# Kernel tuning notes

Hardware: AMD Instinct MI355X
Metric: run time of the kernel (lower is better)

Reference implementation:

```python
import jax, jax.numpy as jnp
import numpy as np


def _conv(x, w, b, stride, pad):
    y = jax.lax.conv_general_dilated(
        x, w, window_strides=(stride, stride),
        padding=((pad, pad), (pad, pad)),
        dimension_numbers=('NCHW', 'OIHW', 'NCHW'))
    return y + b[None, :, None, None]


def setup_inputs() -> dict:
    key = jax.random.key(0)
    ks = jax.random.split(key, 10)
    B, C, H, W = 4, 3, 256, 256
    HID, D, K = 128, 32, 65536
    s = 0.05
    return {
        'x': jax.random.normal(ks[0], (B, C, H, W), dtype=jnp.float32),
        'w1': jax.random.normal(ks[1], (HID, C, 4, 4), dtype=jnp.float32) * s,
        'b1': jnp.zeros((HID,), dtype=jnp.float32),
        'w2': jax.random.normal(ks[2], (HID, HID, 4, 4), dtype=jnp.float32) * s,
        'b2': jnp.zeros((HID,), dtype=jnp.float32),
        'w3': jax.random.normal(ks[3], (HID, HID, 4, 4), dtype=jnp.float32) * s,
        'b3': jnp.zeros((HID,), dtype=jnp.float32),
        'w4': jax.random.normal(ks[4], (D, HID, 3, 3), dtype=jnp.float32) * s,
        'b4': jnp.zeros((D,), dtype=jnp.float32),
        'codebook': jax.random.normal(ks[5], (K, D), dtype=jnp.float32),
    }


def reference(x, w1, b1, w2, b2, w3, b3, w4, b4, codebook):
    z = jax.nn.relu(_conv(x, w1, b1, 2, 1))
    z = jax.nn.relu(_conv(z, w2, b2, 2, 1))
    z = jax.nn.relu(_conv(z, w3, b3, 2, 1))
    z = _conv(z, w4, b4, 1, 1)                 # [B, D, h, w]
    z = jnp.transpose(z, (0, 2, 3, 1))          # [B, h, w, D]
    B, h, w, D = z.shape
    zf = z.reshape(-1, D)                        # [N, D]
    # pairwise squared distances: ||z||^2 + ||e||^2 - 2 z.e
    d = (jnp.sum(zf * zf, axis=1, keepdims=True)
         + jnp.sum(codebook * codebook, axis=1)[None, :]
         - 2.0 * jnp.matmul(zf, codebook.T))    # [N, K]
    idx = jnp.argmin(d, axis=1)                  # [N]
    z_q = codebook[idx].reshape(B, h, w, D)
    return idx.reshape(B, h, w), z_q
```

## Files before the change

kernel.cpp:

```cpp
#include <hip/hip_runtime.h>
#include <cfloat>

typedef float f32x4 __attribute__((ext_vector_type(4)));
typedef _Float16 h8 __attribute__((ext_vector_type(8)));

static __device__ __forceinline__ unsigned umin_(unsigned a, unsigned b) { return a < b ? a : b; }
static __device__ __forceinline__ unsigned umax_(unsigned a, unsigned b) { return a > b ? a : b; }
static __device__ __forceinline__ unsigned med3_(unsigned a, unsigned b, unsigned c) {
    unsigned d;
    asm("v_med3_u32 %0, %1, %2, %3" : "=v"(d) : "v"(a), "v"(b), "v"(c));
    return d;
}

static __device__ __forceinline__ void gl_lds16(const h8* g, h8* s) {
    __builtin_amdgcn_global_load_lds(
        (const __attribute__((address_space(1))) unsigned int*)g,
        (__attribute__((address_space(3))) unsigned int*)s, 16, 0, 0);
}


__global__ __launch_bounds__(256)
void zero_b_k(_Float16* p0, _Float16* p1, _Float16* p2, _Float16* p3,
              _Float16* p4, _Float16* p5) {
    const int s = blockIdx.y;
    _Float16* p; int np, P;
    switch (s) {
        case 0: p = p0; np = 16; P = 66; break;
        case 1: p = p1; np = 16; P = 66; break;
        case 2: p = p2; np = 16; P = 34; break;
        case 3: p = p3; np = 16; P = 34; break;
        case 4: p = p4; np = 4;  P = 34; break;
        default: p = p5; np = 4; P = 34; break;
    }
    const int plane = blockIdx.x;
    if (plane >= np) return;
    _Float16* pl = p + (size_t)plane * P * P * 128;
    const int rowN = P * 128;
    for (int i = threadIdx.x; i < rowN; i += 256) {
        pl[i] = (_Float16)0.f;
        pl[(size_t)(P - 1) * rowN + i] = (_Float16)0.f;
        const int r = i >> 7, c = i & 127;
        pl[(size_t)r * rowN + c] = (_Float16)0.f;
        pl[(size_t)r * rowN + (P - 1) * 128 + c] = (_Float16)0.f;
    }
}

__global__ __launch_bounds__(256)
void conv1_k(const float* __restrict__ in, const float* __restrict__ w,
             const float* __restrict__ bias,
             _Float16* __restrict__ Dh, _Float16* __restrict__ Dl) {
    __shared__ float tile[3][34 * 36];
    const int tid = threadIdx.x;
    const int tx = tid & 15, ty = tid >> 4;
    const int bx = blockIdx.x & 7, by = blockIdx.x >> 3;
    const int oc0 = blockIdx.y * 8;
    const int b = blockIdx.z;
    const int ox = bx * 16 + tx, oy = by * 16 + ty;
    const int ix0 = bx * 32 - 1, iy0 = by * 32 - 1;

    for (int f = tid; f < 3 * 34 * 34; f += 256) {
        const int ic = f / 1156, r2 = f % 1156;
        const int r = r2 / 34, c = r2 % 34;
        const int iy = iy0 + r, ix = ix0 + c;
        float v = ((unsigned)iy < 256u && (unsigned)ix < 256u)
                      ? in[((size_t)(b * 3 + ic) * 256 + iy) * 256 + ix] : 0.f;
        tile[ic][r * 36 + c] = v;
    }
    __syncthreads();

    float acc[8];
#pragma unroll
    for (int j = 0; j < 8; ++j) acc[j] = 0.f;
#pragma unroll
    for (int ic = 0; ic < 3; ++ic) {
#pragma unroll
        for (int kh = 0; kh < 4; ++kh) {
            const float2* p = (const float2*)&tile[ic][(2 * ty + kh) * 36 + 2 * tx];
            const float2 r0 = p[0], r1 = p[1];
            const float tap[4] = {r0.x, r0.y, r1.x, r1.y};
#pragma unroll
            for (int kw = 0; kw < 4; ++kw)
#pragma unroll
                for (int j = 0; j < 8; ++j)
                    acc[j] = fmaf(tap[kw], w[((oc0 + j) * 3 + ic) * 16 + kh * 4 + kw], acc[j]);
        }
    }

    h8 hv, lv;
#pragma unroll
    for (int j = 0; j < 8; ++j) {
        float r = fmaxf(acc[j] + bias[oc0 + j], 0.f);
        _Float16 h = (_Float16)r;
        hv[j] = h;
        lv[j] = (_Float16)((r - (float)h) * 2048.f);
    }
    const size_t di = (((size_t)((b * 2 + (oy & 1)) * 2 + (ox & 1)) * 66 + 1 + (oy >> 1)) * 66
                       + 1 + (ox >> 1)) * 128 + oc0;
    *(h8*)(Dh + di) = hv;
    *(h8*)(Dl + di) = lv;
}

__global__ __launch_bounds__(256)
void pack3_k(const float* __restrict__ w2, const float* __restrict__ w3,
             const float* __restrict__ w4,
             h8* __restrict__ B2h, h8* __restrict__ B2l,
             h8* __restrict__ B3h, h8* __restrict__ B3l,
             h8* __restrict__ B4h, h8* __restrict__ B4l) {
    const float* w; h8 *Bh, *Bl; int T, NT, KHKW;
    switch (blockIdx.y) {
        case 0:  w = w2; Bh = B2h; Bl = B2l; T = 16; NT = 8; KHKW = 16; break;
        case 1:  w = w3; Bh = B3h; Bl = B3l; T = 16; NT = 8; KHKW = 16; break;
        default: w = w4; Bh = B4h; Bl = B4l; T = 9;  NT = 2; KHKW = 9;  break;
    }
    const int idx = blockIdx.x * 256 + threadIdx.x;
    if (idx >= T * 4 * NT * 64) return;
    const int lane = idx & 63;
    int r = idx >> 6;
    const int nt = r % NT; r /= NT;
    const int ks = r & 3;  r >>= 2;
    const int t = r;
    const int oc = nt * 16 + (lane & 15);
    const int icb = ks * 32 + (lane >> 4) * 8;
    h8 hv, lv;
#pragma unroll
    for (int j = 0; j < 8; ++j) {
        const float v = w[(size_t)(oc * 128 + icb + j) * KHKW + t];
        _Float16 h = (_Float16)v;
        hv[j] = h;
        lv[j] = (_Float16)((v - (float)h) * 2048.f);
    }
    Bh[idx] = hv;
    Bl[idx] = lv;
}

template<int WN, bool SPLIT>
__global__ __launch_bounds__(256)
void gemmS2_k(const _Float16* __restrict__ Ah, const _Float16* __restrict__ Al,
              const h8* __restrict__ Bh, const h8* __restrict__ Bl,
              const float* __restrict__ bias,
              _Float16* __restrict__ Dh, _Float16* __restrict__ Dl,
              int OW, int OH, int PP, int dPP) {
    constexpr int NW_N = 8 / WN;
    constexpr int NW_M = 4 / NW_N;
    __shared__ h8 lH[2048];
    __shared__ h8 lL[2048];

    const int tid = threadIdx.x, wid = tid >> 6, l = tid & 63;
    const int nq = wid % NW_N, mi = wid / NW_N;
    const int mt = blockIdx.x * NW_M + mi;
    const int mpr = OW >> 4, mpi = OH * mpr;
    const int b = mt / mpi;
    const int rem = mt % mpi;
    const int oy = rem / mpr, ox = (rem % mpr) << 4;
    const int laneA = (l & 15) * 128 + (l >> 4) * 8;

    f32x4 a1[WN], am[WN];
#pragma unroll
    for (int s = 0; s < WN; ++s) {
        a1[s] = (f32x4){0.f, 0.f, 0.f, 0.f};
        am[s] = (f32x4){0.f, 0.f, 0.f, 0.f};
    }

#pragma unroll 1
    for (int t = 0; t < 16; ++t) {
        {
            const h8* sh = Bh + (size_t)t * 2048 + wid * 512 + l;
            const h8* sl = Bl + (size_t)t * 2048 + wid * 512 + l;
#pragma unroll
            for (int i = 0; i < 8; ++i)
                gl_lds16(sh + i * 64, &lH[wid * 512 + i * 64]);
#pragma unroll
            for (int i = 0; i < 8; ++i)
                gl_lds16(sl + i * 64, &lL[wid * 512 + i * 64]);
        }
        const int kh = t >> 2, kw = t & 3;
        const int dy = (kh - 1) >> 1, dx = (kw - 1) >> 1;
        const int py = (kh - 1) & 1, px = (kw - 1) & 1;
        const int pidx = (b * 2 + py) * 2 + px;
        const size_t abase = ((size_t)(pidx * PP + (oy + dy + 1)) * PP
                              + (ox + dx + 1)) * 128 + laneA;
        h8 avh[4], avl[4];
#pragma unroll
        for (int ks = 0; ks < 4; ++ks) {
            avh[ks] = *(const h8*)(Ah + abase + ks * 32);
            avl[ks] = *(const h8*)(Al + abase + ks * 32);
        }
        __syncthreads();
#pragma unroll
        for (int ks = 0; ks < 4; ++ks) {
#pragma unroll
            for (int s = 0; s < WN; ++s) {
                const h8 bvh = lH[(ks * 8 + nq * WN + s) * 64 + l];
                const h8 bvl = lL[(ks * 8 + nq * WN + s) * 64 + l];
                a1[s] = __builtin_amdgcn_mfma_f32_16x16x32_f16(avh[ks], bvh, a1[s], 0, 0, 0);
                am[s] = __builtin_amdgcn_mfma_f32_16x16x32_f16(avh[ks], bvl, am[s], 0, 0, 0);
                am[s] = __builtin_amdgcn_mfma_f32_16x16x32_f16(avl[ks], bvh, am[s], 0, 0, 0);
            }
        }
        __syncthreads();
    }

#pragma unroll
    for (int s = 0; s < WN; ++s) {
        const int oc = (nq * WN + s) * 16 + (l & 15);
        const float bv = bias[oc];
#pragma unroll
        for (int i = 0; i < 4; ++i) {
            const int row = (l >> 4) * 4 + i;
            float v = fmaf(am[s][i], 4.8828125e-4f, a1[s][i]);
            v = fmaxf(v + bv, 0.f);
            _Float16 h = (_Float16)v;
            _Float16 lo = (_Float16)((v - (float)h) * 2048.f);
            const int oxp = ox + row;
            size_t di;
            if constexpr (SPLIT) {
                di = (((size_t)((b * 2 + (oy & 1)) * 2 + (oxp & 1)) * dPP
                       + 1 + (oy >> 1)) * dPP + 1 + (oxp >> 1)) * 128 + oc;
            } else {
                di = ((size_t)(b * dPP + 1 + oy) * dPP + 1 + oxp) * 128 + oc;
            }
            Dh[di] = h;
            Dl[di] = lo;
        }
    }
}

template<int S, bool FIN, int WPN, int MT>
__global__ __launch_bounds__(256)
void gemm_k(const _Float16* __restrict__ Ah, const _Float16* __restrict__ Al,
            const h8* __restrict__ Bh, const h8* __restrict__ Bl,
            float* __restrict__ part, const float* __restrict__ bias,
            _Float16* __restrict__ Dh, _Float16* __restrict__ Dl,
            int OW, int OH, int PP, int NT, int TPS, int M, int N, int dPP) {
    const int tid = threadIdx.x, wid = tid >> 6, l = tid & 63;
    const int ntb = wid % WPN;
    const int mt0 = (blockIdx.x * (4 / WPN) + wid / WPN) * MT;
    const int sp = blockIdx.y;
    const int mpr = OW >> 4, mpi = OH * mpr;
    const int laneA = (l & 15) * 128 + (l >> 4) * 8;

    int bmt[MT], oymt[MT], oxmt[MT];
#pragma unroll
    for (int m = 0; m < MT; ++m) {
        const int mt = mt0 + m;
        bmt[m] = mt / mpi;
        const int rem = mt % mpi;
        oymt[m] = rem / mpr;
        oxmt[m] = (rem % mpr) << 4;
    }

    f32x4 a1[MT][2], am[MT][2];
#pragma unroll
    for (int m = 0; m < MT; ++m)
#pragma unroll
        for (int s = 0; s < 2; ++s) {
            a1[m][s] = (f32x4){0.f, 0.f, 0.f, 0.f};
            am[m][s] = (f32x4){0.f, 0.f, 0.f, 0.f};
        }

    const int t0 = sp * TPS, t1 = t0 + TPS;
#pragma unroll 2
    for (int t = t0; t < t1; ++t) {
        int dy, dx, pidx[MT];
        if constexpr (S == 2) {
            const int kh = t >> 2, kw = t & 3;
            dy = (kh - 1) >> 1; dx = (kw - 1) >> 1;
            const int py = (kh - 1) & 1, px = (kw - 1) & 1;
#pragma unroll
            for (int m = 0; m < MT; ++m) pidx[m] = (bmt[m] * 2 + py) * 2 + px;
        } else {
            dy = t / 3 - 1; dx = t % 3 - 1;
#pragma unroll
            for (int m = 0; m < MT; ++m) pidx[m] = bmt[m];
        }
        const _Float16* pAh[MT]; const _Float16* pAl[MT];
#pragma unroll
        for (int m = 0; m < MT; ++m) {
            const size_t base = ((size_t)(pidx[m] * PP + (oymt[m] + dy + 1)) * PP
                                 + (oxmt[m] + dx + 1)) * 128 + laneA;
            pAh[m] = Ah + base;
            pAl[m] = Al + base;
        }
        const size_t bbase = ((size_t)(t * 4) * NT + ntb * 2) * 64 + l;
#pragma unroll
        for (int ks = 0; ks < 4; ++ks) {
            h8 avh[MT], avl[MT];
#pragma unroll
            for (int m = 0; m < MT; ++m) {
                avh[m] = *(const h8*)(pAh[m] + ks * 32);
                avl[m] = *(const h8*)(pAl[m] + ks * 32);
            }
#pragma unroll
            for (int s = 0; s < 2; ++s) {
                const h8 bvh = Bh[bbase + (size_t)ks * NT * 64 + s * 64];
                const h8 bvl = Bl[bbase + (size_t)ks * NT * 64 + s * 64];
#pragma unroll
                for (int m = 0; m < MT; ++m) {
                    a1[m][s] = __builtin_amdgcn_mfma_f32_16x16x32_f16(avh[m], bvh, a1[m][s], 0, 0, 0);
                    am[m][s] = __builtin_amdgcn_mfma_f32_16x16x32_f16(avh[m], bvl, am[m][s], 0, 0, 0);
                    am[m][s] = __builtin_amdgcn_mfma_f32_16x16x32_f16(avl[m], bvh, am[m][s], 0, 0, 0);
                }
            }
        }
    }

#pragma unroll
    for (int m = 0; m < MT; ++m) {
        const int mt = mt0 + m;
#pragma unroll
        for (int s = 0; s < 2; ++s) {
            const int oc = ntb * 32 + s * 16 + (l & 15);
#pragma unroll
            for (int i = 0; i < 4; ++i) {
                const int row = (l >> 4) * 4 + i;
                float v = fmaf(am[m][s][i], 4.8828125e-4f, a1[m][s][i]);
                if (!FIN) {
                    part[((size_t)sp * M + mt * 16 + row) * N + oc] = v;
                } else {
                    v = fmaxf(v + bias[oc], 0.f);
                    _Float16 h = (_Float16)v;
                    _Float16 lo = (_Float16)((v - (float)h) * 2048.f);
                    const int ox = oxmt[m] + row;
                    const int oy = oymt[m], b = bmt[m];
                    const size_t di = (((size_t)((b * 2 + (oy & 1)) * 2 + (ox & 1)) * dPP
                                        + 1 + (oy >> 1)) * dPP + 1 + (ox >> 1)) * 128 + oc;
                    Dh[di] = h;
                    Dl[di] = lo;
                }
            }
        }
    }
}

__global__ __launch_bounds__(256)
void fin4_k(const float* __restrict__ part, const float* __restrict__ bias,
            float* __restrict__ zz, h8* __restrict__ zh, h8* __restrict__ zl) {
    const int t = blockIdx.x * 256 + threadIdx.x;
    const int m = t >> 2, g8 = (t & 3) * 8;
    float v[8];
#pragma unroll
    for (int j = 0; j < 8; ++j) v[j] = bias[g8 + j];
#pragma unroll
    for (int sp = 0; sp < 3; ++sp) {
        const float4* p = (const float4*)(part + ((size_t)sp * 4096 + m) * 32 + g8);
        float4 x0 = p[0], x1 = p[1];
        v[0] += x0.x; v[1] += x0.y; v[2] += x0.z; v[3] += x0.w;
        v[4] += x1.x; v[5] += x1.y; v[6] += x1.z; v[7] += x1.w;
    }
    float4* dst = (float4*)(zz + (size_t)m * 32 + g8);
    dst[0] = make_float4(v[0], v[1], v[2], v[3]);
    dst[1] = make_float4(v[4], v[5], v[6], v[7]);
    h8 hv, lv;
#pragma unroll
    for (int j = 0; j < 8; ++j) {
        const float mv = -2.f * v[j];
        _Float16 h = (_Float16)mv;
        hv[j] = h;
        lv[j] = (_Float16)(mv - (float)h);
    }
    const int idx = (m >> 4) * 64 + (m & 15) + (t & 3) * 16;
    zh[idx] = hv;
    zl[idx] = lv;
}

#define VQ_NSPLIT 64
#define VQ_KSPC   1024
#define VQ_NCHUNK 8
#define VQ_TAU_S  102.4f
#define VQ_ABS_S  524288.0f
#define VQ_QT     4

__global__ __launch_bounds__(256)
void split_cb_k(const float* __restrict__ cb, h8* __restrict__ cbh, h8* __restrict__ cbl,
                float* __restrict__ cbn2, float* __restrict__ cbn_raw,
                unsigned* __restrict__ counter) {
    const int c = blockIdx.x * 256 + threadIdx.x;
    const float4* p = (const float4*)(cb + (size_t)c * 32);
    float e[32];
    float s = 0.f;
#pragma unroll
    for (int i = 0; i < 8; ++i) {
        float4 v = p[i];
        e[i*4+0] = v.x; e[i*4+1] = v.y; e[i*4+2] = v.z; e[i*4+3] = v.w;
        s += v.x*v.x + v.y*v.y + v.z*v.z + v.w*v.w;
    }
    cbn_raw[c] = s;
    cbn2[c]    = (s + 512.0f) * 2048.0f;
    const int base = (c >> 4) * 64 + (c & 15);
#pragma unroll
    for (int g = 0; g < 4; ++g) {
        h8 hv, lv;
#pragma unroll
        for (int j = 0; j < 8; ++j) {
            float v = e[g*8 + j];
            _Float16 h = (_Float16)v;
            hv[j] = (_Float16)((float)h * 2048.0f);
            lv[j] = (_Float16)((v - (float)h) * 2048.0f);
        }
        cbh[base + g*16] = hv;
        cbl[base + g*16] = lv;
    }
    if (c == 0) *counter = 0u;
}

__global__ __launch_bounds__(256, 4)
void vq_mfma_k(const h8* __restrict__ zh, const h8* __restrict__ zl,
               const uint4* __restrict__ cbh, const uint4* __restrict__ cbl,
               const float* __restrict__ cbn2,
               unsigned* __restrict__ pb1, unsigned* __restrict__ pb2,
               unsigned* __restrict__ pcol) {
    __shared__ uint4 lH[2][512];
    __shared__ uint4 lL[2][512];
    __shared__ float lN[2][128];

    const int tid = threadIdx.x;
    const int w = tid >> 6, ln = tid & 63;
    const int split = blockIdx.y;
    const int qt0 = (blockIdx.x * 4 + w) * VQ_QT;

    h8 azh[VQ_QT], azl[VQ_QT];
#pragma unroll
    for (int qq = 0; qq < VQ_QT; ++qq) {
        azh[qq] = zh[(qt0 + qq) * 64 + ln];
        azl[qq] = zl[(qt0 + qq) * 64 + ln];
    }

    unsigned b1[VQ_QT][4], b2[VQ_QT][4];
#pragma unroll
    for (int qq = 0; qq < VQ_QT; ++qq)
#pragma unroll
        for (int i = 0; i < 4; ++i) { b1[qq][i] = 0x7F800000u; b2[qq][i] = 0x7F800000u; }

    const int fbase = split * (VQ_KSPC * 4);
    const int nbase = split * VQ_KSPC;

    {
        uint4 h0 = cbh[fbase + tid], h1 = cbh[fbase + 256 + tid];
        uint4 l0 = cbl[fbase + tid], l1 = cbl[fbase + 256 + tid];
        lH[0][tid] = h0; lH[0][tid + 256] = h1;
        lL[0][tid] = l0; lL[0][tid + 256] = l1;
        if (tid < 128) lN[0][tid] = cbn2[nbase + tid];
    }
    __syncthreads();

    for (int ci = 0; ci < VQ_NCHUNK; ++ci) {
        const int cur = ci & 1;
        const bool more = (ci + 1 < VQ_NCHUNK);
        uint4 nh0, nh1, nl0, nl1; float nn = 0.f;
        if (more) {
            const int nb = fbase + (ci + 1) * 512;
            nh0 = cbh[nb + tid]; nh1 = cbh[nb + 256 + tid];
            nl0 = cbl[nb + tid]; nl1 = cbl[nb + 256 + tid];
            if (tid < 128) nn = cbn2[nbase + (ci + 1) * 128 + tid];
        }

        const unsigned tcb = (unsigned)(ci * 8);
#pragma unroll
        for (int t = 0; t < 8; ++t) {
            const h8 bh = *reinterpret_cast<const h8*>(&lH[cur][t*64 + ln]);
            const h8 bl = *reinterpret_cast<const h8*>(&lL[cur][t*64 + ln]);
            const float nv = lN[cur][t*16 + (ln & 15)];
            f32x4 nvv = {nv, nv, nv, nv};
            const unsigned tc = tcb + t;
#pragma unroll
            for (int qq = 0; qq < VQ_QT; ++qq) {
                f32x4 acc;
                acc = __builtin_amdgcn_mfma_f32_16x16x32_f16(azh[qq], bh, nvv, 0, 0, 0);
                acc = __builtin_amdgcn_mfma_f32_16x16x32_f16(azh[qq], bl, acc, 0, 0, 0);
                acc = __builtin_amdgcn_mfma_f32_16x16x32_f16(azl[qq], bh, acc, 0, 0, 0);
#pragma unroll
                for (int i = 0; i < 4; ++i) {
                    const unsigned k0 = (__float_as_uint(acc[i]) & 0xFFFFFF00u) | tc;
                    b2[qq][i] = med3_(b1[qq][i], b2[qq][i], k0);
                    b1[qq][i] = umin_(b1[qq][i], k0);
                }
            }
        }

        if (more) {
            const int nxt = cur ^ 1;
            lH[nxt][tid] = nh0; lH[nxt][tid + 256] = nh1;
            lL[nxt][tid] = nl0; lL[nxt][tid + 256] = nl1;
            if (tid < 128) lN[nxt][tid] = nn;
        }
        __syncthreads();
    }

#pragma unroll
    for (int qq = 0; qq < VQ_QT; ++qq) {
#pragma unroll
        for (int i = 0; i < 4; ++i) {
            unsigned v1 = b1[qq][i], v2 = b2[qq][i], cv = (unsigned)(ln & 15);
#pragma unroll
            for (int m = 1; m < 16; m <<= 1) {
                unsigned o1 = __shfl_xor(v1, m, 64);
                unsigned o2 = __shfl_xor(v2, m, 64);
                unsigned oc = __shfl_xor(cv, m, 64);
                unsigned nb2 = umin_(umin_(v2, o2), umax_(v1, o1));
                if (o1 < v1) cv = oc;
                v1 = umin_(v1, o1); v2 = nb2;
            }
            if ((ln & 15) == 0) {
                const int q = (qt0 + qq) * 16 + (ln >> 4) * 4 + i;
                pb1[(size_t)q * VQ_NSPLIT + split] = v1;
                pb2[(size_t)q * VQ_NSPLIT + split] = v2;
                pcol[(size_t)q * VQ_NSPLIT + split] = cv;
            }
        }
    }
}

__global__ __launch_bounds__(256)
void combine_k(const unsigned* __restrict__ pb1, const unsigned* __restrict__ pb2,
               const unsigned* __restrict__ pcol,
               unsigned* __restrict__ coarse, unsigned* __restrict__ flags,
               unsigned* __restrict__ list, unsigned* __restrict__ counter) {
    const int q = blockIdx.x * 256 + threadIdx.x;
    unsigned B1 = 0x7F800000u, B2 = 0x7F800000u, PAY = 0u;
#pragma unroll 4
    for (int s = 0; s < VQ_NSPLIT; ++s) {
        unsigned a1 = pb1[(size_t)q * VQ_NSPLIT + s];
        unsigned a2 = pb2[(size_t)q * VQ_NSPLIT + s];
        unsigned ac = pcol[(size_t)q * VQ_NSPLIT + s];
        unsigned nb2 = umin_(umin_(B2, a2), umax_(B1, a1));
        if (a1 < B1) PAY = ((unsigned)s << 4) | ac;
        B1 = umin_(B1, a1); B2 = nb2;
    }
    const unsigned tile = B1 & 0xFFu;
    const unsigned code = (PAY >> 4) * VQ_KSPC + tile * 16 + (PAY & 15u);
    const float f1 = __uint_as_float(B1 & 0xFFFFFF00u);
    const float f2 = __uint_as_float(B2 & 0xFFFFFF00u);
    const int fl = (f2 - f1 < VQ_TAU_S) || (f1 < VQ_ABS_S);
    coarse[q] = code;
    flags[q] = (unsigned)fl;
    if (fl) { unsigned p = atomicAdd(counter, 1u); list[p] = q; }
}

__global__ __launch_bounds__(256)
void guard_k(const float* __restrict__ cb, const float* __restrict__ cbn_raw,
             const float* __restrict__ zz, const unsigned* __restrict__ list,
             const unsigned* __restrict__ counter, float2* __restrict__ gpart) {
    __shared__ float lcb[256 * 36];
    __shared__ float lnr[256];
    __shared__ float2 red[4];
    __shared__ int ns;

    const int tid = threadIdx.x;
    const int w = tid >> 6, ln = tid & 63;
    const int bx = blockIdx.x;

    const float4* cb4 = (const float4*)cb;
#pragma unroll
    for (int it = 0; it < 8; ++it) {
        const int f = tid + it * 256;
        float4 v = cb4[(size_t)bx * 2048 + f];
        const int c = f >> 3, g = f & 7;
        *(float4*)&lcb[c * 36 + g * 4] = v;
    }
    lnr[tid] = cbn_raw[bx * 256 + tid];
    if (tid == 0) ns = (int)*(volatile unsigned*)counter;
    __syncthreads();

    for (int ii = blockIdx.y; ii < ns; ii += 8) {
        const int q = (int)list[ii];
        const float4* zq = (const float4*)(zz + (size_t)q * 32);
        float m2[32];
#pragma unroll
        for (int j = 0; j < 8; ++j) {
            float4 v = zq[j];
            m2[j*4+0] = -2.f*v.x; m2[j*4+1] = -2.f*v.y; m2[j*4+2] = -2.f*v.z; m2[j*4+3] = -2.f*v.w;
        }
        float d = lnr[tid];
#pragma unroll
        for (int j = 0; j < 8; ++j) {
            float4 e = *(const float4*)&lcb[tid * 36 + j * 4];
            d = fmaf(m2[j*4+0], e.x, d);
            d = fmaf(m2[j*4+1], e.y, d);
            d = fmaf(m2[j*4+2], e.z, d);
            d = fmaf(m2[j*4+3], e.w, d);
        }
        float bv = d; int bc = tid;
#pragma unroll
        for (int m = 1; m < 64; m <<= 1) {
            float ov = __shfl_xor(bv, m, 64);
            int   oi = __shfl_xor(bc, m, 64);
            if (ov < bv || (ov == bv && oi < bc)) { bv = ov; bc = oi; }
        }
        if (ln == 0) red[w] = make_float2(bv, (float)(bx * 256 + bc));
        __syncthreads();
        if (tid == 0) {
            float2 r = red[0];
#pragma unroll
            for (int k = 1; k < 4; ++k) {
                float2 o = red[k];
                if (o.x < r.x || (o.x == r.x && o.y < r.y)) r = o;
            }
            gpart[(size_t)q * 256 + bx] = r;
        }
        __syncthreads();
    }
}

__global__ __launch_bounds__(256)
void final_k(const unsigned* __restrict__ flags, const unsigned* __restrict__ coarse,
             const float2* __restrict__ gpart, const float* __restrict__ cb,
             float* __restrict__ out_idx, float* __restrict__ out_zq) {
    const int q = blockIdx.x * 256 + threadIdx.x;
    int bi;
    if (flags[q]) {
        float2 r = gpart[(size_t)q * 256];
        for (int b = 1; b < 256; ++b) {
            float2 o = gpart[(size_t)q * 256 + b];
            if (o.x < r.x || (o.x == r.x && o.y < r.y)) r = o;
        }
        bi = (int)r.y;
    } else {
        bi = (int)coarse[q];
    }
    out_idx[q] = (float)bi;
    const float4* src = (const float4*)(cb + (size_t)bi * 32);
    float4*       dst = (float4*)(out_zq + (size_t)q * 32);
#pragma unroll
    for (int i = 0; i < 8; ++i) dst[i] = src[i];
}

extern "C" void kernel_launch(void* const* d_in, const int* in_sizes, int n_in,
                              void* d_out, int out_size, void* d_ws, size_t ws_size,
                              hipStream_t stream) {
    const float* x  = (const float*)d_in[0];
    const float* w1 = (const float*)d_in[1];
    const float* b1 = (const float*)d_in[2];
    const float* w2 = (const float*)d_in[3];
    const float* b2 = (const float*)d_in[4];
    const float* w3 = (const float*)d_in[5];
    const float* b3 = (const float*)d_in[6];
    const float* w4 = (const float*)d_in[7];
    const float* b4 = (const float*)d_in[8];
    const float* cb = (const float*)d_in[9];
    float* out = (float*)d_out;

    float* ws = (float*)d_ws;
    _Float16* y1h = (_Float16*)ws;
    _Float16* y1l = (_Float16*)(ws + 4460544);
    _Float16* y2h = (_Float16*)(ws + 8921088);
    _Float16* y2l = (_Float16*)(ws + 10104832);
    _Float16* y3h = (_Float16*)(ws + 11288576);
    _Float16* y3l = (_Float16*)(ws + 11584512);
    float* zzp = ws + 11880448;
    h8* B2h = (h8*)(ws + 12011520);
    h8* B2l = (h8*)(ws + 12142592);
    h8* B3h = (h8*)(ws + 12273664);
    h8* B3l = (h8*)(ws + 12404736);
    h8* B4h = (h8*)(ws + 12535808);
    h8* B4l = (h8*)(ws + 12554240);
    float* part = ws + 12572672;
    h8*       cbh     = (h8*)ws;
    h8*       cbl     = (h8*)(ws + 1048576);
    h8*       zh      = (h8*)(ws + 2097152);
    h8*       zl      = (h8*)(ws + 2162688);
    float*    cbn2    = ws + 2228224;
    float*    cbn_raw = ws + 2293760;
    unsigned* pb1     = (unsigned*)(ws + 2359296);
    unsigned* pb2     = (unsigned*)(ws + 2621440);
    unsigned* pcol    = (unsigned*)(ws + 2883584);
    unsigned* coarse  = (unsigned*)(ws + 3145728);
    unsigned* flags   = (unsigned*)(ws + 3149824);
    unsigned* list    = (unsigned*)(ws + 3153920);
    unsigned* counter = (unsigned*)(ws + 3158016);
    float2*   gpart   = (float2*)(ws + 3158080);

    zero_b_k<<<dim3(16, 6), 256, 0, stream>>>(y1h, y1l, y2h, y2l, y3h, y3l);
    pack3_k<<<dim3(128, 3), 256, 0, stream>>>(w2, w3, w4, B2h, B2l, B3h, B3l, B4h, B4l);
    conv1_k<<<dim3(64, 16, 4), 256, 0, stream>>>(x, w1, b1, y1h, y1l);
    gemmS2_k<4, true><<<dim3(512), 256, 0, stream>>>(y1h, y1l, B2h, B2l, b2, y2h, y2l,
                                                     64, 64, 66, 34);
    gemmS2_k<2, false><<<dim3(256), 256, 0, stream>>>(y2h, y2l, B3h, B3l, b3, y3h, y3l,
                                                      32, 32, 34, 34);
    gemm_k<1, false, 1, 1><<<dim3(64, 3), 256, 0, stream>>>(y3h, y3l, B4h, B4l, part, nullptr, nullptr, nullptr,
                                                            32, 32, 34, 2, 3, 4096, 32, 0);
    fin4_k<<<64, 256, 0, stream>>>(part, b4, zzp, zh, zl);

    split_cb_k<<<256, 256, 0, stream>>>(cb, cbh, cbl, cbn2, cbn_raw, counter);
    vq_mfma_k <<<dim3(16, VQ_NSPLIT), 256, 0, stream>>>(zh, zl, (const uint4*)cbh, (const uint4*)cbl,
                                                        cbn2, pb1, pb2, pcol);
    combine_k <<<16,  256, 0, stream>>>(pb1, pb2, pcol, coarse, flags, list, counter);
    guard_k   <<<dim3(256, 8), 256, 0, stream>>>(cb, cbn_raw, zzp, list, counter, gpart);
    final_k   <<<16,  256, 0, stream>>>(flags, coarse, gpart, cb, out, out + 4096);
}
```

Measured before the change: 276.5 us.

## Double-buffer weight tiles in LDS and add M-tiling to stride-2 conv GEMM

The stride-2 convolution GEMM kernel now double-buffers the per-tap weight tiles in LDS, prefetching tap t+1 with async global-to-LDS loads while MFMAs run on tap t. This removes one barrier per iteration. A new MT template parameter lets each wave compute several M tiles, so every B fragment read from LDS is reused across them; the first conv GEMM uses MT=2 with half as many blocks. In exchange the kernel uses twice the LDS and more registers, and launch_bounds(256,1) may reduce occupancy.

New measurement: 277.5 us. Within noise of the previous version (+0.4%).

```diff
diff --git a/kernel.cpp b/kernel.cpp
--- a/kernel.cpp
+++ b/kernel.cpp
@@ -133,8 +133,8 @@
     Bl[idx] = lv;
 }
 
-template<int WN, bool SPLIT>
-__global__ __launch_bounds__(256)
+template<int WN, int MT, bool SPLIT>
+__global__ __launch_bounds__(256, 1)
 void gemmS2_k(const _Float16* __restrict__ Ah, const _Float16* __restrict__ Al,
               const h8* __restrict__ Bh, const h8* __restrict__ Bl,
               const float* __restrict__ bias,
@@ -142,85 +142,113 @@
               int OW, int OH, int PP, int dPP) {
     constexpr int NW_N = 8 / WN;
     constexpr int NW_M = 4 / NW_N;
-    __shared__ h8 lH[2048];
-    __shared__ h8 lL[2048];
+    __shared__ h8 lH[2][2048];
+    __shared__ h8 lL[2][2048];
 
     const int tid = threadIdx.x, wid = tid >> 6, l = tid & 63;
     const int nq = wid % NW_N, mi = wid / NW_N;
-    const int mt = blockIdx.x * NW_M + mi;
+    const int mt0 = (blockIdx.x * NW_M + mi) * MT;
     const int mpr = OW >> 4, mpi = OH * mpr;
-    const int b = mt / mpi;
-    const int rem = mt % mpi;
-    const int oy = rem / mpr, ox = (rem % mpr) << 4;
     const int laneA = (l & 15) * 128 + (l >> 4) * 8;
 
-    f32x4 a1[WN], am[WN];
-#pragma unroll
-    for (int s = 0; s < WN; ++s) {
-        a1[s] = (f32x4){0.f, 0.f, 0.f, 0.f};
-        am[s] = (f32x4){0.f, 0.f, 0.f, 0.f};
-    }
+    int bm[MT], oym[MT], oxm[MT];
+#pragma unroll
+    for (int m = 0; m < MT; ++m) {
+        const int mt = mt0 + m;
+        bm[m] = mt / mpi;
+        const int rem = mt % mpi;
+        oym[m] = rem / mpr;
+        oxm[m] = (rem % mpr) << 4;
+    }
+
+    f32x4 a1[MT][WN], am[MT][WN];
+#pragma unroll
+    for (int m = 0; m < MT; ++m)
+#pragma unroll
+        for (int s = 0; s < WN; ++s) {
+            a1[m][s] = (f32x4){0.f, 0.f, 0.f, 0.f};
+            am[m][s] = (f32x4){0.f, 0.f, 0.f, 0.f};
+        }
+
+    {
+        const h8* sh = Bh + wid * 512 + l;
+        const h8* sl = Bl + wid * 512 + l;
+#pragma unroll
+        for (int i = 0; i < 8; ++i) gl_lds16(sh + i * 64, &lH[0][wid * 512 + i * 64]);
+#pragma unroll
+        for (int i = 0; i < 8; ++i) gl_lds16(sl + i * 64, &lL[0][wid * 512 + i * 64]);
+    }
+    __syncthreads();
 
 #pragma unroll 1
     for (int t = 0; t < 16; ++t) {
-        {
-            const h8* sh = Bh + (size_t)t * 2048 + wid * 512 + l;
-            const h8* sl = Bl + (size_t)t * 2048 + wid * 512 + l;
-#pragma unroll
-            for (int i = 0; i < 8; ++i)
-                gl_lds16(sh + i * 64, &lH[wid * 512 + i * 64]);
-#pragma unroll
-            for (int i = 0; i < 8; ++i)
-                gl_lds16(sl + i * 64, &lL[wid * 512 + i * 64]);
-        }
+        const int cur = t & 1;
         const int kh = t >> 2, kw = t & 3;
         const int dy = (kh - 1) >> 1, dx = (kw - 1) >> 1;
         const int py = (kh - 1) & 1, px = (kw - 1) & 1;
-        const int pidx = (b * 2 + py) * 2 + px;
-        const size_t abase = ((size_t)(pidx * PP + (oy + dy + 1)) * PP
-                              + (ox + dx + 1)) * 128 + laneA;
-        h8 avh[4], avl[4];
+        h8 avh[MT][4], avl[MT][4];
+#pragma unroll
+        for (int m = 0; m < MT; ++m) {
+            const int pidx = (bm[m] * 2 + py) * 2 + px;
+            const size_t abase = ((size_t)(pidx * PP + (oym[m] + dy + 1)) * PP
+                                  + (oxm[m] + dx + 1)) * 128 + laneA;
+#pragma unroll
+            for (int ks = 0; ks < 4; ++ks) {
+                avh[m][ks] = *(const h8*)(Ah + abase + ks * 32);
+                avl[m][ks] = *(const h8*)(Al + abase + ks * 32);
+            }
+        }
+        if (t + 1 < 16) {
+            const int nxt = cur ^ 1;
+            const h8* sh = Bh + (size_t)(t + 1) * 2048 + wid * 512 + l;
+            const h8* sl = Bl + (size_t)(t + 1) * 2048 + wid * 512 + l;
+#pragma unroll
+            for (int i = 0; i < 8; ++i) gl_lds16(sh + i * 64, &lH[nxt][wid * 512 + i * 64]);
+#pragma unroll
+            for (int i = 0; i < 8; ++i) gl_lds16(sl + i * 64, &lL[nxt][wid * 512 + i * 64]);
+        }
 #pragma unroll
         for (int ks = 0; ks < 4; ++ks) {
-            avh[ks] = *(const h8*)(Ah + abase + ks * 32);
-            avl[ks] = *(const h8*)(Al + abase + ks * 32);
+#pragma unroll
+            for (int s = 0; s < WN; ++s) {
+                const h8 bvh = lH[cur][(ks * 8 + nq * WN + s) * 64 + l];
+                const h8 bvl = lL[cur][(ks * 8 + nq * WN + s) * 64 + l];
+#pragma unroll
+                for (int m = 0; m < MT; ++m) {
+                    a1[m][s] = __builtin_amdgcn_mfma_f32_16x16x32_f16(avh[m][ks], bvh, a1[m][s], 0, 0, 0);
+                    am[m][s] = __builtin_amdgcn_mfma_f32_16x16x32_f16(avh[m][ks], bvl, am[m][s], 0, 0, 0);
+                    am[m][s] = __builtin_amdgcn_mfma_f32_16x16x32_f16(avl[m][ks], bvh, am[m][s], 0, 0, 0);
+                }
+            }
         }
         __syncthreads();
-#pragma unroll
-        for (int ks = 0; ks < 4; ++ks) {
-#pragma unroll
-            for (int s = 0; s < WN; ++s) {
-                const h8 bvh = lH[(ks * 8 + nq * WN + s) * 64 + l];
-                const h8 bvl = lL[(ks * 8 + nq * WN + s) * 64 + l];
-                a1[s] = __builtin_amdgcn_mfma_f32_16x16x32_f16(avh[ks], bvh, a1[s], 0, 0, 0);
-                am[s] = __builtin_amdgcn_mfma_f32_16x16x32_f16(avh[ks], bvl, am[s], 0, 0, 0);
-                am[s] = __builtin_amdgcn_mfma_f32_16x16x32_f16(avl[ks], bvh, am[s], 0, 0, 0);
-            }
-        }
-        __syncthreads();
-    }
-
-#pragma unroll
-    for (int s = 0; s < WN; ++s) {
-        const int oc = (nq * WN + s) * 16 + (l & 15);
-        const float bv = bias[oc];
-#pragma unroll
-        for (int i = 0; i < 4; ++i) {
-            const int row = (l >> 4) * 4 + i;
-            float v = fmaf(am[s][i], 4.8828125e-4f, a1[s][i]);
-            v = fmaxf(v + bv, 0.f);
-            _Float16 h = (_Float16)v;
-            _Float16 lo = (_Float16)((v - (float)h) * 2048.f);
-            const int oxp = ox + row;
-            size_t di;
-            if constexpr (SPLIT) {
-                di = (((size_t)((b * 2 + (oy & 1)) * 2 + (oxp & 1)) * dPP
-                       + 1 + (oy >> 1)) * dPP + 1 + (oxp >> 1)) * 128 + oc;
-            } else {
-                di = ((size_t)(b * dPP + 1 + oy) * dPP + 1 + oxp) * 128 + oc;
-            }
-            Dh[di] = h;
-            Dl[di] = lo;
+    }
+
+#pragma unroll
+    for (int m = 0; m < MT; ++m) {
+#pragma unroll
+        for (int s = 0; s < WN; ++s) {
+            const int oc = (nq * WN + s) * 16 + (l & 15);
+            const float bv = bias[oc];
+#pragma unroll
+            for (int i = 0; i < 4; ++i) {
+                const int row = (l >> 4) * 4 + i;
+                float v = fmaf(am[m][s][i], 4.8828125e-4f, a1[m][s][i]);
+                v = fmaxf(v + bv, 0.f);
+                _Float16 h = (_Float16)v;
+                _Float16 lo = (_Float16)((v - (float)h) * 2048.f);
+                const int oxp = oxm[m] + row;
+                const int oy = oym[m], b = bm[m];
+                size_t di;
+                if constexpr (SPLIT) {
+                    di = (((size_t)((b * 2 + (oy & 1)) * 2 + (oxp & 1)) * dPP
+                           + 1 + (oy >> 1)) * dPP + 1 + (oxp >> 1)) * 128 + oc;
+                } else {
+                    di = ((size_t)(b * dPP + 1 + oy) * dPP + 1 + oxp) * 128 + oc;
+                }
+                Dh[di] = h;
+                Dl[di] = lo;
+            }
         }
     }
 }
@@ -672,10 +700,10 @@
     zero_b_k<<<dim3(16, 6), 256, 0, stream>>>(y1h, y1l, y2h, y2l, y3h, y3l);
     pack3_k<<<dim3(128, 3), 256, 0, stream>>>(w2, w3, w4, B2h, B2l, B3h, B3l, B4h, B4l);
     conv1_k<<<dim3(64, 16, 4), 256, 0, stream>>>(x, w1, b1, y1h, y1l);
-    gemmS2_k<4, true><<<dim3(512), 256, 0, stream>>>(y1h, y1l, B2h, B2l, b2, y2h, y2l,
-                                                     64, 64, 66, 34);
-    gemmS2_k<2, false><<<dim3(256), 256, 0, stream>>>(y2h, y2l, B3h, B3l, b3, y3h, y3l,
-                                                      32, 32, 34, 34);
+    gemmS2_k<4, 2, true><<<dim3(256), 256, 0, stream>>>(y1h, y1l, B2h, B2l, b2, y2h, y2l,
+                                                        64, 64, 66, 34);
+    gemmS2_k<2, 1, false><<<dim3(256), 256, 0, stream>>>(y2h, y2l, B3h, B3l, b3, y3h, y3l,
+                                                         32, 32, 34, 34);
     gemm_k<1, false, 1, 1><<<dim3(64, 3), 256, 0, stream>>>(y3h, y3l, B4h, B4l, part, nullptr, nullptr, nullptr,
                                                             32, 32, 34, 2, 3, 4096, 32, 0);
     fin4_k<<<64, 256, 0, stream>>>(part, b4, zzp, zh, zl);
```

## Register-prefetch conv weight tiles, per-wave guard queries, wave-parallel final reduction

Applied to the files above, without the earlier changes.

The stride-2 conv GEMM kernels stop using direct global-to-LDS loads issued each tap. Instead they prefetch the next tap's weight tile into registers while the current tap's MFMAs run, then write it to LDS behind a barrier, so weight loads overlap compute. The guard kernel now handles one flagged query per wave instead of one per block, which removes the LDS reduction and two block barriers per query. The final kernel reduces the 256 partials per query with a wave shuffle instead of a serial per-thread loop, at the cost of more register pressure and extra LDS stores in the GEMM.

Result: faster. 251.9 us (-8.9%).

```diff
diff --git a/kernel.cpp b/kernel.cpp
--- a/kernel.cpp
+++ b/kernel.cpp
@@ -10,12 +10,6 @@
     unsigned d;
     asm("v_med3_u32 %0, %1, %2, %3" : "=v"(d) : "v"(a), "v"(b), "v"(c));
     return d;
-}
-
-static __device__ __forceinline__ void gl_lds16(const h8* g, h8* s) {
-    __builtin_amdgcn_global_load_lds(
-        (const __attribute__((address_space(1))) unsigned int*)g,
-        (__attribute__((address_space(3))) unsigned int*)s, 16, 0, 0);
 }
 
 
@@ -135,11 +129,11 @@
 
 template<int WN, bool SPLIT>
 __global__ __launch_bounds__(256)
-void gemmS2_k(const _Float16* __restrict__ Ah, const _Float16* __restrict__ Al,
-              const h8* __restrict__ Bh, const h8* __restrict__ Bl,
-              const float* __restrict__ bias,
-              _Float16* __restrict__ Dh, _Float16* __restrict__ Dl,
-              int OW, int OH, int PP, int dPP) {
+void gemmP_k(const _Float16* __restrict__ Ah, const _Float16* __restrict__ Al,
+             const h8* __restrict__ Bh, const h8* __restrict__ Bl,
+             const float* __restrict__ bias,
+             _Float16* __restrict__ Dh, _Float16* __restrict__ Dl,
+             int OW, int OH, int PP, int dPP) {
     constexpr int NW_N = 8 / WN;
     constexpr int NW_M = 4 / NW_N;
     __shared__ h8 lH[2048];
@@ -161,18 +155,21 @@
         am[s] = (f32x4){0.f, 0.f, 0.f, 0.f};
     }
 
+    h8 rh[8], rl[8];
+#pragma unroll
+    for (int i = 0; i < 8; ++i) {
+        rh[i] = Bh[i * 256 + tid];
+        rl[i] = Bl[i * 256 + tid];
+    }
+#pragma unroll
+    for (int i = 0; i < 8; ++i) {
+        lH[i * 256 + tid] = rh[i];
+        lL[i * 256 + tid] = rl[i];
+    }
+    __syncthreads();
+
 #pragma unroll 1
     for (int t = 0; t < 16; ++t) {
-        {
-            const h8* sh = Bh + (size_t)t * 2048 + wid * 512 + l;
-            const h8* sl = Bl + (size_t)t * 2048 + wid * 512 + l;
-#pragma unroll
-            for (int i = 0; i < 8; ++i)
-                gl_lds16(sh + i * 64, &lH[wid * 512 + i * 64]);
-#pragma unroll
-            for (int i = 0; i < 8; ++i)
-                gl_lds16(sl + i * 64, &lL[wid * 512 + i * 64]);
-        }
         const int kh = t >> 2, kw = t & 3;
         const int dy = (kh - 1) >> 1, dx = (kw - 1) >> 1;
         const int py = (kh - 1) & 1, px = (kw - 1) & 1;
@@ -185,7 +182,15 @@
             avh[ks] = *(const h8*)(Ah + abase + ks * 32);
             avl[ks] = *(const h8*)(Al + abase + ks * 32);
         }
-        __syncthreads();
+        if (t + 1 < 16) {
+            const h8* sh = Bh + (size_t)(t + 1) * 2048;
+            const h8* sl = Bl + (size_t)(t + 1) * 2048;
+#pragma unroll
+            for (int i = 0; i < 8; ++i) {
+                rh[i] = sh[i * 256 + tid];
+                rl[i] = sl[i * 256 + tid];
+            }
+        }
 #pragma unroll
         for (int ks = 0; ks < 4; ++ks) {
 #pragma unroll
@@ -198,6 +203,14 @@
             }
         }
         __syncthreads();
+        if (t + 1 < 16) {
+#pragma unroll
+            for (int i = 0; i < 8; ++i) {
+                lH[i * 256 + tid] = rh[i];
+                lL[i * 256 + tid] = rl[i];
+            }
+            __syncthreads();
+        }
     }
 
 #pragma unroll
@@ -542,7 +555,6 @@
              const unsigned* __restrict__ counter, float2* __restrict__ gpart) {
     __shared__ float lcb[256 * 36];
     __shared__ float lnr[256];
-    __shared__ float2 red[4];
     __shared__ int ns;
 
     const int tid = threadIdx.x;
@@ -561,7 +573,7 @@
     if (tid == 0) ns = (int)*(volatile unsigned*)counter;
     __syncthreads();
 
-    for (int ii = blockIdx.y; ii < ns; ii += 8) {
+    for (int ii = blockIdx.y * 4 + w; ii < ns; ii += 32) {
         const int q = (int)list[ii];
         const float4* zq = (const float4*)(zz + (size_t)q * 32);
         float m2[32];
@@ -570,34 +582,28 @@
             float4 v = zq[j];
             m2[j*4+0] = -2.f*v.x; m2[j*4+1] = -2.f*v.y; m2[j*4+2] = -2.f*v.z; m2[j*4+3] = -2.f*v.w;
         }
-        float d = lnr[tid];
-#pragma unroll
-        for (int j = 0; j < 8; ++j) {
-            float4 e = *(const float4*)&lcb[tid * 36 + j * 4];
-            d = fmaf(m2[j*4+0], e.x, d);
-            d = fmaf(m2[j*4+1], e.y, d);
-            d = fmaf(m2[j*4+2], e.z, d);
-            d = fmaf(m2[j*4+3], e.w, d);
-        }
-        float bv = d; int bc = tid;
+        float bv = FLT_MAX; int bc = 0x7FFFFFFF;
+#pragma unroll
+        for (int cc = 0; cc < 4; ++cc) {
+            const int c = cc * 64 + ln;
+            float d = lnr[c];
+#pragma unroll
+            for (int j = 0; j < 8; ++j) {
+                float4 e = *(const float4*)&lcb[c * 36 + j * 4];
+                d = fmaf(m2[j*4+0], e.x, d);
+                d = fmaf(m2[j*4+1], e.y, d);
+                d = fmaf(m2[j*4+2], e.z, d);
+                d = fmaf(m2[j*4+3], e.w, d);
+            }
+            if (d < bv || (d == bv && c < bc)) { bv = d; bc = c; }
+        }
 #pragma unroll
         for (int m = 1; m < 64; m <<= 1) {
             float ov = __shfl_xor(bv, m, 64);
             int   oi = __shfl_xor(bc, m, 64);
             if (ov < bv || (ov == bv && oi < bc)) { bv = ov; bc = oi; }
         }
-        if (ln == 0) red[w] = make_float2(bv, (float)(bx * 256 + bc));
-        __syncthreads();
-        if (tid == 0) {
-            float2 r = red[0];
-#pragma unroll
-            for (int k = 1; k < 4; ++k) {
-                float2 o = red[k];
-                if (o.x < r.x || (o.x == r.x && o.y < r.y)) r = o;
-            }
-            gpart[(size_t)q * 256 + bx] = r;
-        }
-        __syncthreads();
+        if (ln == 0) gpart[(size_t)q * 256 + bx] = make_float2(bv, (float)(bx * 256 + bc));
     }
 }
 
@@ -605,23 +611,33 @@
 void final_k(const unsigned* __restrict__ flags, const unsigned* __restrict__ coarse,
              const float2* __restrict__ gpart, const float* __restrict__ cb,
              float* __restrict__ out_idx, float* __restrict__ out_zq) {
-    const int q = blockIdx.x * 256 + threadIdx.x;
+    const int tid = threadIdx.x, w = tid >> 6, ln = tid & 63;
+    const int q = blockIdx.x * 4 + w;
     int bi;
     if (flags[q]) {
-        float2 r = gpart[(size_t)q * 256];
-        for (int b = 1; b < 256; ++b) {
+        float bv = FLT_MAX; int bidx = 0x7FFFFFFF;
+#pragma unroll
+        for (int k = 0; k < 4; ++k) {
+            const int b = k * 64 + ln;
             float2 o = gpart[(size_t)q * 256 + b];
-            if (o.x < r.x || (o.x == r.x && o.y < r.y)) r = o;
-        }
-        bi = (int)r.y;
+            int oi = (int)o.y;
+            if (o.x < bv || (o.x == bv && oi < bidx)) { bv = o.x; bidx = oi; }
+        }
+#pragma unroll
+        for (int m = 1; m < 64; m <<= 1) {
+            float ov = __shfl_xor(bv, m, 64);
+            int   oi = __shfl_xor(bidx, m, 64);
+            if (ov < bv || (ov == bv && oi < bidx)) { bv = ov; bidx = oi; }
+        }
+        bi = bidx;
     } else {
         bi = (int)coarse[q];
     }
-    out_idx[q] = (float)bi;
-    const float4* src = (const float4*)(cb + (size_t)bi * 32);
-    float4*       dst = (float4*)(out_zq + (size_t)q * 32);
-#pragma unroll
-    for (int i = 0; i < 8; ++i) dst[i] = src[i];
+    if (ln == 0) out_idx[q] = (float)bi;
+    if (ln < 8) {
+        float4 v = ((const float4*)(cb + (size_t)bi * 32))[ln];
+        ((float4*)(out_zq + (size_t)q * 32))[ln] = v;
+    }
 }
 
 extern "C" void kernel_launch(void* const* d_in, const int* in_sizes, int n_in,
@@ -672,10 +688,10 @@
     zero_b_k<<<dim3(16, 6), 256, 0, stream>>>(y1h, y1l, y2h, y2l, y3h, y3l);
     pack3_k<<<dim3(128, 3), 256, 0, stream>>>(w2, w3, w4, B2h, B2l, B3h, B3l, B4h, B4l);
     conv1_k<<<dim3(64, 16, 4), 256, 0, stream>>>(x, w1, b1, y1h, y1l);
-    gemmS2_k<4, true><<<dim3(512), 256, 0, stream>>>(y1h, y1l, B2h, B2l, b2, y2h, y2l,
-                                                     64, 64, 66, 34);
-    gemmS2_k<2, false><<<dim3(256), 256, 0, stream>>>(y2h, y2l, B3h, B3l, b3, y3h, y3l,
-                                                      32, 32, 34, 34);
+    gemmP_k<4, true><<<dim3(512), 256, 0, stream>>>(y1h, y1l, B2h, B2l, b2, y2h, y2l,
+                                                    64, 64, 66, 34);
+    gemmP_k<2, false><<<dim3(256), 256, 0, stream>>>(y2h, y2l, B3h, B3l, b3, y3h, y3l,
+                                                     32, 32, 34, 34);
     gemm_k<1, false, 1, 1><<<dim3(64, 3), 256, 0, stream>>>(y3h, y3l, B4h, B4l, part, nullptr, nullptr, nullptr,
                                                             32, 32, 34, 2, 3, 4096, 32, 0);
     fin4_k<<<64, 256, 0, stream>>>(part, b4, zzp, zh, zl);
@@ -685,5 +701,5 @@
                                                         cbn2, pb1, pb2, pcol);
     combine_k <<<16,  256, 0, stream>>>(pb1, pb2, pcol, coarse, flags, list, counter);
     guard_k   <<<dim3(256, 8), 256, 0, stream>>>(cb, cbn_raw, zzp, list, counter, gpart);
-    final_k   <<<16,  256, 0, stream>>>(flags, coarse, gpart, cb, out, out + 4096);
-}
+    final_k   <<<1024, 256, 0, stream>>>(flags, coarse, gpart, cb, out, out + 4096);
+}
```
